# Optimization experiments

Hardware: AMD Instinct MI355X
Metric: run time of the kernel (lower is better)

Reference implementation:

```python
import jax, jax.numpy as jnp
import numpy as np

B, N = 32, 512            # batch, max nodes per graph
F_DIM, M_DIM = 1024, 256  # node feature dim, first hidden dim
N_SEM = 8                 # number of semantic-class experts
XYZ, DIM_E = 3, 8
OUT_SIZE = 2 * XYZ + DIM_E  # 14 (default reg branch)
EPS = 1e-8                # padding value used by out_seq_to_batch


def setup_inputs() -> dict:
    key = jax.random.key(0)
    ks = jax.random.split(key, 12)
    def w(k, shape, fan_in):
        return jax.random.normal(k, shape, jnp.float32) / np.float32(np.sqrt(fan_in))
    return {
        "nodes": jax.random.normal(ks[0], (B, N, F_DIM), jnp.float32),
        "sem": jax.random.randint(ks[1], (B, N), 0, N_SEM, jnp.int32),
        "lengths": jax.random.randint(ks[2], (B,), 64, N + 1, jnp.int32),
        # y expert MLPs (4 layers), stacked over experts
        "W1": w(ks[3], (N_SEM, F_DIM, M_DIM), F_DIM), "b1": jnp.zeros((N_SEM, M_DIM), jnp.float32),
        "W2": w(ks[4], (N_SEM, M_DIM, 64), M_DIM),   "b2": jnp.zeros((N_SEM, 64), jnp.float32),
        "W3": w(ks[5], (N_SEM, 64, 32), 64),         "b3": jnp.zeros((N_SEM, 32), jnp.float32),
        "W4": w(ks[6], (N_SEM, 32, OUT_SIZE), 32),   "b4": jnp.zeros((N_SEM, OUT_SIZE), jnp.float32),
        # rot expert MLPs (2 layers), stacked over experts
        "R1": w(ks[7], (N_SEM, F_DIM, M_DIM), F_DIM), "rb1": jnp.zeros((N_SEM, M_DIM), jnp.float32),
        "R2": w(ks[8], (N_SEM, M_DIM, XYZ), M_DIM),   "rb2": jnp.zeros((N_SEM, XYZ), jnp.float32),
    }


def _prim_mlps(nodes, sem, lengths, W1, b1, W2, b2, W3, b3, W4, b4, R1, rb1, R2, rb2):
    Bn, Nn, Fd = nodes.shape
    x = nodes.reshape(-1, Fd)                       # [T, F], T = B*N tokens
    semf = sem.reshape(-1)                          # [T] expert id per token
    # dense dispatch: run every expert on all tokens, then select per token
    h1 = jax.nn.relu(jnp.einsum('tf,efm->etm', x, W1) + b1[:, None, :])   # [E,T,M]
    h2 = jax.nn.relu(jnp.einsum('etm,emh->eth', h1, W2) + b2[:, None, :]) # [E,T,64]
    h3 = jax.nn.relu(jnp.einsum('eth,ehg->etg', h2, W3) + b3[:, None, :]) # [E,T,32]
    y_all = jnp.einsum('etg,ego->eto', h3, W4) + b4[:, None, :]           # [E,T,OUT]
    r1 = jax.nn.relu(jnp.einsum('tf,efm->etm', x, R1) + rb1[:, None, :])  # [E,T,M]
    rot_all = jnp.einsum('etm,emo->eto', r1, R2) + rb2[:, None, :]        # [E,T,XYZ]
    t = jnp.arange(x.shape[0])
    y = y_all[semf, t]                              # [T, OUT]
    rot = rot_all[semf, t]                          # [T, XYZ]
    out = jnp.concatenate([y, rot], axis=-1).reshape(Bn, Nn, -1)
    # positions beyond each graph's length are filled with eps (out_seq_to_batch)
    mask = (jnp.arange(Nn)[None, :] < lengths[:, None])[:, :, None]
    return jnp.where(mask, out, jnp.float32(EPS))


def reference(nodes, sem, lengths, W1, b1, W2, b2, W3, b3, W4, b4, R1, rb1, R2, rb2):
    return _prim_mlps(nodes, sem, lengths, W1, b1, W2, b2, W3, b3, W4, b4,
                      R1, rb1, R2, rb2)
```

## Files before the change

### kernel.cpp

```cpp
#include <hip/hip_runtime.h>
#include <stdint.h>

#define T_TOK 16384
#define NE 8
#define EPSV 1e-8f
#define MAXC128 136
#define MAXC64  264

#define WS_PERM   0
#define WS_CNT    65536
#define WS_CUR    65600
#define WS_OFFS   65664
#define WS_XS     131072
#define WS_WT     (WS_XS + 16512*1024*2)
#define WS_H1     (WS_WT + 8*512*1024*2)
#define WS_W2T    (WS_H1 + 16448*512*2)
#define WS_W3T    (WS_W2T + 8*64*256*2)
#define WS_W4T    (WS_W3T + 8*32*64*2)
#define WS_R2T    (WS_W4T + 8*16*32*2)

typedef __attribute__((ext_vector_type(8))) short bf16x8;
typedef __attribute__((ext_vector_type(4))) float f32x4;

__device__ __forceinline__ unsigned short f2bf(float f) {
    unsigned u = __float_as_uint(f);
    u += 0x7fffu + ((u >> 16) & 1u);
    return (unsigned short)(u >> 16);
}
__device__ __forceinline__ float bf2f(unsigned short h) {
    return __uint_as_float(((unsigned)h) << 16);
}

__device__ __forceinline__ void gl_lds16(const void* g, void* l) {
    __builtin_amdgcn_global_load_lds(
        (const __attribute__((address_space(1))) void*)g,
        (__attribute__((address_space(3))) void*)l,
        16, 0, 0);
}

__device__ __forceinline__ bool chunk_lookup(const int* __restrict__ offs, int c, int csize,
                                             int& e, int& base, int& len) {
    int acc = 0;
#pragma unroll
    for (int i = 0; i < NE; i++) {
        int s = offs[i], t = offs[i + 1];
        int cc = (t - s + csize - 1) / csize;
        if (c < acc + cc) {
            e = i;
            base = s + (c - acc) * csize;
            len = (t - base < csize) ? (t - base) : csize;
            return true;
        }
        acc += cc;
    }
    return false;
}

__global__ __launch_bounds__(64) void k_zero(int* __restrict__ ws_i) {
    int t = threadIdx.x;
    if (t < NE) ws_i[(WS_CNT >> 2) + t] = 0;
    if (t < NE) ws_i[(WS_CUR >> 2) + t] = 0;
}

__global__ __launch_bounds__(256) void k_hist(const int* __restrict__ sem, int* __restrict__ ws_i) {
    __shared__ int cnt[NE];
    int tid = threadIdx.x, lane = tid & 63;
    if (tid < NE) cnt[tid] = 0;
    __syncthreads();
    int s = sem[blockIdx.x * 256 + tid];
#pragma unroll
    for (int e = 0; e < NE; e++) {
        unsigned long long m = __ballot(s == e);
        if (lane == e) atomicAdd(&cnt[e], (int)__popcll(m));
    }
    __syncthreads();
    if (tid < NE) atomicAdd(ws_i + (WS_CNT >> 2) + tid, cnt[tid]);
}

__global__ __launch_bounds__(64) void k_scan(int* __restrict__ ws_i) {
    if (threadIdx.x == 0) {
        int acc = 0;
        int* offs = ws_i + (WS_OFFS >> 2);
        for (int e = 0; e < NE; e++) {
            offs[e] = acc;
            ws_i[(WS_CUR >> 2) + e] = acc;
            acc += ws_i[(WS_CNT >> 2) + e];
        }
        offs[NE] = acc;
    }
}

__global__ __launch_bounds__(256) void k_scatter(const int* __restrict__ sem, int* __restrict__ ws_i) {
    int tid = threadIdx.x, lane = tid & 63;
    int i = blockIdx.x * 256 + tid;
    int s = sem[i];
    int* perm = ws_i + (WS_PERM >> 2);
#pragma unroll
    for (int e = 0; e < NE; e++) {
        unsigned long long m = __ballot(s == e);
        if (s == e) {
            int leader = (int)__builtin_ctzll(m);
            int rank = (int)__popcll(m & ((1ull << lane) - 1ull));
            int bpos = 0;
            if (lane == leader) bpos = atomicAdd(ws_i + (WS_CUR >> 2) + e, (int)__popcll(m));
            bpos = __shfl(bpos, leader, 64);
            perm[bpos + rank] = i;
        }
    }
}

__global__ __launch_bounds__(256) void k_xgather(const float* __restrict__ x,
                                                 const int* __restrict__ perm,
                                                 unsigned short* __restrict__ xs) {
    int gid = blockIdx.x * 256 + threadIdx.x;
    int st = gid >> 7;
    int k8 = gid & 127;
    int src = perm[st];
    const float4* p = (const float4*)(x + (size_t)src * 1024 + k8 * 8);
    float4 a = p[0], b = p[1];
    unsigned r0 = (unsigned)f2bf(a.x) | ((unsigned)f2bf(a.y) << 16);
    unsigned r1 = (unsigned)f2bf(a.z) | ((unsigned)f2bf(a.w) << 16);
    unsigned r2 = (unsigned)f2bf(b.x) | ((unsigned)f2bf(b.y) << 16);
    unsigned r3 = (unsigned)f2bf(b.z) | ((unsigned)f2bf(b.w) << 16);
    *(uint4*)(xs + (size_t)st * 1024 + k8 * 8) = make_uint4(r0, r1, r2, r3);
}

__global__ __launch_bounds__(256) void k_wcvt(const float* __restrict__ W1,
                                              const float* __restrict__ R1,
                                              unsigned short* __restrict__ wt) {
    __shared__ float tile[64][65];
    int k0 = blockIdx.x * 64;
    int n0 = blockIdx.y * 64;
    int e  = blockIdx.z;
    const float* src = (n0 < 256) ? (W1 + (size_t)e * 1024 * 256 + n0)
                                  : (R1 + (size_t)e * 1024 * 256 + (n0 - 256));
    int tid = threadIdx.x;
    int rr = tid >> 4;
    int cg = (tid & 15) * 4;
#pragma unroll
    for (int p = 0; p < 4; p++) {
        int kk = p * 16 + rr;
        float4 v = *(const float4*)(src + (size_t)(k0 + kk) * 256 + cg);
        tile[kk][cg] = v.x; tile[kk][cg + 1] = v.y; tile[kk][cg + 2] = v.z; tile[kk][cg + 3] = v.w;
    }
    __syncthreads();
    int nn = tid >> 3;
    int k8 = tid & 7;
#pragma unroll
    for (int p = 0; p < 2; p++) {
        int n = p * 32 + nn;
        unsigned w[4];
#pragma unroll
        for (int j = 0; j < 4; j++) {
            float f0 = tile[k8 * 8 + 2 * j][n];
            float f1 = tile[k8 * 8 + 2 * j + 1][n];
            w[j] = (unsigned)f2bf(f0) | ((unsigned)f2bf(f1) << 16);
        }
        *(uint4*)(wt + (size_t)(e * 512 + n0 + n) * 1024 + k0 + k8 * 8) =
            make_uint4(w[0], w[1], w[2], w[3]);
    }
}

__global__ __launch_bounds__(256) void k_wcvt2(const float* __restrict__ W2,
                                               const float* __restrict__ W3,
                                               const float* __restrict__ W4,
                                               const float* __restrict__ R2,
                                               unsigned short* __restrict__ w2t,
                                               unsigned short* __restrict__ w3t,
                                               unsigned short* __restrict__ w4t,
                                               unsigned short* __restrict__ r2t) {
    int e = blockIdx.x, t = threadIdx.x;
    for (int idx = t; idx < 64 * 256; idx += 256) {
        int k = idx & 255, n = idx >> 8;
        w2t[(size_t)(e * 64 + n) * 256 + k] = f2bf(W2[(size_t)e * 16384 + k * 64 + n]);
    }
    for (int idx = t; idx < 32 * 64; idx += 256) {
        int k = idx & 63, n = idx >> 6;
        w3t[(size_t)(e * 32 + n) * 64 + k] = f2bf(W3[(size_t)e * 2048 + k * 32 + n]);
    }
    for (int idx = t; idx < 16 * 32; idx += 256) {
        int k = idx & 31, n = idx >> 5;
        w4t[(size_t)(e * 16 + n) * 32 + k] = (n < 14) ? f2bf(W4[(size_t)e * 448 + k * 14 + n])
                                                      : (unsigned short)0;
    }
    for (int idx = t; idx < 16 * 256; idx += 256) {
        int k = idx & 255, n = idx >> 8;
        r2t[(size_t)(e * 16 + n) * 256 + k] = (n < 3) ? f2bf(R2[(size_t)e * 768 + k * 3 + n])
                                                      : (unsigned short)0;
    }
}

__global__ __launch_bounds__(256) void k_gemm(const unsigned short* __restrict__ xs,
                                              const unsigned short* __restrict__ wt,
                                              const float* __restrict__ b1,
                                              const float* __restrict__ rb1,
                                              const int* __restrict__ ws_i,
                                              unsigned short* __restrict__ h1) {
    __shared__ __align__(16) short As[128 * 32];
    __shared__ __align__(16) short Bs[128 * 32];
    int e, base, len;
    if (!chunk_lookup(ws_i + (WS_OFFS >> 2), blockIdx.x, 128, e, base, len)) return;
    int n0 = blockIdx.y * 128;
    int tid = threadIdx.x;
    int wave = tid >> 6, lane = tid & 63;
    int quad = lane >> 4, lr = lane & 15;
    int wm = (wave & 1) * 64, wn = (wave >> 1) * 64;

    f32x4 acc[4][4];
#pragma unroll
    for (int i = 0; i < 4; i++)
#pragma unroll
        for (int j = 0; j < 4; j++) acc[i][j] = (f32x4){0.f, 0.f, 0.f, 0.f};

    const unsigned short* Ag = xs + (size_t)base * 1024;
    const unsigned short* Bg = wt + (size_t)(e * 512 + n0) * 1024;

    for (int kb = 0; kb < 32; kb++) {
        __syncthreads();
#pragma unroll
        for (int i = 0; i < 2; i++) {
            int g = i * 256 + wave * 64 + lane;
            int r = g >> 2, k8 = g & 3;
            gl_lds16(Ag + (size_t)r * 1024 + kb * 32 + k8 * 8,
                     As + (size_t)(i * 256 + wave * 64) * 8);
            gl_lds16(Bg + (size_t)r * 1024 + kb * 32 + k8 * 8,
                     Bs + (size_t)(i * 256 + wave * 64) * 8);
        }
        __syncthreads();

        bf16x8 af[4], bfr[4];
#pragma unroll
        for (int im = 0; im < 4; im++)
            af[im] = *(const bf16x8*)(As + ((wm + im * 16 + lr) * 32 + quad * 8));
#pragma unroll
        for (int in = 0; in < 4; in++)
            bfr[in] = *(const bf16x8*)(Bs + ((wn + in * 16 + lr) * 32 + quad * 8));
#pragma unroll
        for (int im = 0; im < 4; im++)
#pragma unroll
            for (int in = 0; in < 4; in++)
                acc[im][in] = __builtin_amdgcn_mfma_f32_16x16x32_bf16(af[im], bfr[in], acc[im][in], 0, 0, 0);
    }

#pragma unroll
    for (int in = 0; in < 4; in++) {
        int gcol = n0 + wn + in * 16 + lr;
        float bias = (gcol < 256) ? b1[e * 256 + gcol] : rb1[e * 256 + gcol - 256];
#pragma unroll
        for (int im = 0; im < 4; im++) {
#pragma unroll
            for (int v = 0; v < 4; v++) {
                int r = wm + im * 16 + quad * 4 + v;
                if (r < len) {
                    float val = fmaxf(acc[im][in][v] + bias, 0.f);
                    h1[(size_t)(base + r) * 512 + gcol] = f2bf(val);
                }
            }
        }
    }
}

__global__ __launch_bounds__(256) void k_tail(const unsigned short* __restrict__ h1,
                                              const int* __restrict__ ws_i,
                                              const unsigned short* __restrict__ w2t,
                                              const unsigned short* __restrict__ w3t,
                                              const unsigned short* __restrict__ w4t,
                                              const unsigned short* __restrict__ r2t,
                                              const float* __restrict__ b2,
                                              const float* __restrict__ b3,
                                              const float* __restrict__ b4,
                                              const float* __restrict__ rb2,
                                              const int* __restrict__ lengths,
                                              float* __restrict__ out) {
    __shared__ __align__(16) unsigned short h2s[4][16][64];
    __shared__ __align__(16) unsigned short h3s[4][16][32];

    int e, base, len;
    if (!chunk_lookup(ws_i + (WS_OFFS >> 2), blockIdx.x, 64, e, base, len)) return;
    int tid = threadIdx.x, wave = tid >> 6, lane = tid & 63;
    int quad = lane >> 4, lr = lane & 15;
    int m0 = wave * 16;

    const unsigned short* Ap = h1 + (size_t)(base + m0) * 512;

    f32x4 acc2[4];
#pragma unroll
    for (int t = 0; t < 4; t++) {
        float bb = b2[e * 64 + t * 16 + lr];
        acc2[t] = (f32x4){bb, bb, bb, bb};
    }
    f32x4 accr;
    { float bb = (lr < 3) ? rb2[e * 3 + lr] : 0.f; accr = (f32x4){bb, bb, bb, bb}; }

    const unsigned short* W2e = w2t + (size_t)e * 64 * 256;
    const unsigned short* R2e = r2t + (size_t)e * 16 * 256;
#pragma unroll
    for (int kk = 0; kk < 8; kk++) {
        int k0 = kk * 32;
        bf16x8 a = *(const bf16x8*)(Ap + lr * 512 + k0 + quad * 8);
#pragma unroll
        for (int t = 0; t < 4; t++) {
            bf16x8 b = *(const bf16x8*)(W2e + (t * 16 + lr) * 256 + k0 + quad * 8);
            acc2[t] = __builtin_amdgcn_mfma_f32_16x16x32_bf16(a, b, acc2[t], 0, 0, 0);
        }
        bf16x8 ar = *(const bf16x8*)(Ap + lr * 512 + 256 + k0 + quad * 8);
        bf16x8 br = *(const bf16x8*)(R2e + lr * 256 + k0 + quad * 8);
        accr = __builtin_amdgcn_mfma_f32_16x16x32_bf16(ar, br, accr, 0, 0, 0);
    }
#pragma unroll
    for (int t = 0; t < 4; t++)
#pragma unroll
        for (int v = 0; v < 4; v++)
            h2s[wave][quad * 4 + v][t * 16 + lr] = f2bf(fmaxf(acc2[t][v], 0.f));

    f32x4 acc3[2];
#pragma unroll
    for (int t = 0; t < 2; t++) {
        float bb = b3[e * 32 + t * 16 + lr];
        acc3[t] = (f32x4){bb, bb, bb, bb};
    }
    const unsigned short* W3e = w3t + (size_t)e * 32 * 64;
#pragma unroll
    for (int kk = 0; kk < 2; kk++) {
        int k0 = kk * 32;
        bf16x8 a = *(const bf16x8*)(&h2s[wave][lr][k0 + quad * 8]);
#pragma unroll
        for (int t = 0; t < 2; t++) {
            bf16x8 b = *(const bf16x8*)(W3e + (t * 16 + lr) * 64 + k0 + quad * 8);
            acc3[t] = __builtin_amdgcn_mfma_f32_16x16x32_bf16(a, b, acc3[t], 0, 0, 0);
        }
    }
#pragma unroll
    for (int t = 0; t < 2; t++)
#pragma unroll
        for (int v = 0; v < 4; v++)
            h3s[wave][quad * 4 + v][t * 16 + lr] = f2bf(fmaxf(acc3[t][v], 0.f));

    f32x4 acc4;
    { float bb = (lr < 14) ? b4[e * 14 + lr] : 0.f; acc4 = (f32x4){bb, bb, bb, bb}; }
    {
        bf16x8 a = *(const bf16x8*)(&h3s[wave][lr][quad * 8]);
        bf16x8 b = *(const bf16x8*)(w4t + ((size_t)e * 16 + lr) * 32 + quad * 8);
        acc4 = __builtin_amdgcn_mfma_f32_16x16x32_bf16(a, b, acc4, 0, 0, 0);
    }

    const int* perm = ws_i + (WS_PERM >> 2);
#pragma unroll
    for (int v = 0; v < 4; v++) {
        int t = m0 + quad * 4 + v;
        if (t < len) {
            int token = perm[base + t];
            int bi = token >> 9, ni = token & 511;
            int valid = ni < lengths[bi];
            if (lr < 14) out[(size_t)token * 17 + lr] = valid ? acc4[v] : EPSV;
            if (lr < 3)  out[(size_t)token * 17 + 14 + lr] = valid ? accr[v] : EPSV;
        }
    }
}

extern "C" void kernel_launch(void* const* d_in, const int* in_sizes, int n_in,
                              void* d_out, int out_size, void* d_ws, size_t ws_size,
                              hipStream_t stream) {
    (void)in_sizes; (void)n_in; (void)out_size; (void)ws_size;
    const float* nodes   = (const float*)d_in[0];
    const int*   sem     = (const int*)d_in[1];
    const int*   lengths = (const int*)d_in[2];
    const float* W1 = (const float*)d_in[3];
    const float* b1 = (const float*)d_in[4];
    const float* W2 = (const float*)d_in[5];
    const float* b2 = (const float*)d_in[6];
    const float* W3 = (const float*)d_in[7];
    const float* b3 = (const float*)d_in[8];
    const float* W4 = (const float*)d_in[9];
    const float* b4 = (const float*)d_in[10];
    const float* R1  = (const float*)d_in[11];
    const float* rb1 = (const float*)d_in[12];
    const float* R2  = (const float*)d_in[13];
    const float* rb2 = (const float*)d_in[14];
    float* out = (float*)d_out;

    char* ws = (char*)d_ws;
    int* ws_i = (int*)ws;
    unsigned short* xs  = (unsigned short*)(ws + WS_XS);
    unsigned short* wt  = (unsigned short*)(ws + WS_WT);
    unsigned short* h1  = (unsigned short*)(ws + WS_H1);
    unsigned short* w2t = (unsigned short*)(ws + WS_W2T);
    unsigned short* w3t = (unsigned short*)(ws + WS_W3T);
    unsigned short* w4t = (unsigned short*)(ws + WS_W4T);
    unsigned short* r2t = (unsigned short*)(ws + WS_R2T);

    hipLaunchKernelGGL(k_zero, dim3(1), dim3(64), 0, stream, ws_i);
    hipLaunchKernelGGL(k_hist, dim3(64), dim3(256), 0, stream, sem, ws_i);
    hipLaunchKernelGGL(k_scan, dim3(1), dim3(64), 0, stream, ws_i);
    hipLaunchKernelGGL(k_scatter, dim3(64), dim3(256), 0, stream, sem, ws_i);
    hipLaunchKernelGGL(k_xgather, dim3(8192), dim3(256), 0, stream, nodes, (const int*)ws_i, xs);
    hipLaunchKernelGGL(k_wcvt, dim3(16, 8, 8), dim3(256), 0, stream, W1, R1, wt);
    hipLaunchKernelGGL(k_wcvt2, dim3(8), dim3(256), 0, stream, W2, W3, W4, R2, w2t, w3t, w4t, r2t);
    hipLaunchKernelGGL(k_gemm, dim3(MAXC128, 4), dim3(256), 0, stream,
                       (const unsigned short*)xs, (const unsigned short*)wt, b1, rb1,
                       (const int*)ws_i, h1);
    hipLaunchKernelGGL(k_tail, dim3(MAXC64), dim3(256), 0, stream,
                       (const unsigned short*)h1, (const int*)ws_i,
                       (const unsigned short*)w2t, (const unsigned short*)w3t,
                       (const unsigned short*)w4t, (const unsigned short*)r2t,
                       b2, b3, b4, rb2, lengths, out);
}
```

Before: 236.0 us.

## Cut launches via per-block hist partials, fuse weight converts, widen GEMM K tile

Per-block histogram partials are written out, and each scatter block computes its own expert offsets from them. This removes the zero and scan kernels and the global atomics on cursors. The small-weight conversion is folded into the W1/R1 conversion kernel, spread across its blocks, so one more launch goes away. The first-layer GEMM now loads 64-wide K tiles with an XOR-swizzled LDS layout, halving the number of K iterations and barriers and reducing bank conflicts, at the cost of doubled LDS per block.

```diff
diff --git a/kernel.cpp b/kernel.cpp
--- a/kernel.cpp
+++ b/kernel.cpp
@@ -8,9 +8,8 @@
 #define MAXC64  264
 
 #define WS_PERM   0
-#define WS_CNT    65536
-#define WS_CUR    65600
-#define WS_OFFS   65664
+#define WS_PART   65536
+#define WS_OFFS   67584
 #define WS_XS     131072
 #define WS_WT     (WS_XS + 16512*1024*2)
 #define WS_H1     (WS_WT + 8*512*1024*2)
@@ -56,12 +55,6 @@
     return false;
 }
 
-__global__ __launch_bounds__(64) void k_zero(int* __restrict__ ws_i) {
-    int t = threadIdx.x;
-    if (t < NE) ws_i[(WS_CNT >> 2) + t] = 0;
-    if (t < NE) ws_i[(WS_CUR >> 2) + t] = 0;
-}
-
 __global__ __launch_bounds__(256) void k_hist(const int* __restrict__ sem, int* __restrict__ ws_i) {
     __shared__ int cnt[NE];
     int tid = threadIdx.x, lane = tid & 63;
@@ -74,25 +67,38 @@
         if (lane == e) atomicAdd(&cnt[e], (int)__popcll(m));
     }
     __syncthreads();
-    if (tid < NE) atomicAdd(ws_i + (WS_CNT >> 2) + tid, cnt[tid]);
-}
-
-__global__ __launch_bounds__(64) void k_scan(int* __restrict__ ws_i) {
-    if (threadIdx.x == 0) {
-        int acc = 0;
-        int* offs = ws_i + (WS_OFFS >> 2);
-        for (int e = 0; e < NE; e++) {
-            offs[e] = acc;
-            ws_i[(WS_CUR >> 2) + e] = acc;
-            acc += ws_i[(WS_CNT >> 2) + e];
-        }
-        offs[NE] = acc;
-    }
+    if (tid < NE) ws_i[(WS_PART >> 2) + blockIdx.x * NE + tid] = cnt[tid];
 }
 
 __global__ __launch_bounds__(256) void k_scatter(const int* __restrict__ sem, int* __restrict__ ws_i) {
-    int tid = threadIdx.x, lane = tid & 63;
-    int i = blockIdx.x * 256 + tid;
+    __shared__ int parts[64 * NE];
+    __shared__ int tot[NE], preb[NE], ebase[NE + 1];
+    __shared__ int cur[NE];
+    int b = blockIdx.x, tid = threadIdx.x, lane = tid & 63;
+    parts[tid] = ws_i[(WS_PART >> 2) + tid];
+    parts[256 + tid] = ws_i[(WS_PART >> 2) + 256 + tid];
+    __syncthreads();
+    if (tid < NE) {
+        int t = 0, p = 0;
+        for (int bb = 0; bb < 64; bb++) {
+            int v = parts[bb * NE + tid];
+            t += v;
+            if (bb < b) p += v;
+        }
+        tot[tid] = t; preb[tid] = p;
+    }
+    __syncthreads();
+    if (tid == 0) {
+        int base = 0;
+        for (int e = 0; e < NE; e++) { ebase[e] = base; base += tot[e]; }
+        ebase[NE] = base;
+        if (b == 0)
+            for (int e = 0; e <= NE; e++) ws_i[(WS_OFFS >> 2) + e] = ebase[e];
+    }
+    __syncthreads();
+    if (tid < NE) cur[tid] = ebase[tid] + preb[tid];
+    __syncthreads();
+    int i = b * 256 + tid;
     int s = sem[i];
     int* perm = ws_i + (WS_PERM >> 2);
 #pragma unroll
@@ -102,7 +108,7 @@
             int leader = (int)__builtin_ctzll(m);
             int rank = (int)__popcll(m & ((1ull << lane) - 1ull));
             int bpos = 0;
-            if (lane == leader) bpos = atomicAdd(ws_i + (WS_CUR >> 2) + e, (int)__popcll(m));
+            if (lane == leader) bpos = atomicAdd(&cur[e], (int)__popcll(m));
             bpos = __shfl(bpos, leader, 64);
             perm[bpos + rank] = i;
         }
@@ -127,7 +133,15 @@
 
 __global__ __launch_bounds__(256) void k_wcvt(const float* __restrict__ W1,
                                               const float* __restrict__ R1,
-                                              unsigned short* __restrict__ wt) {
+                                              const float* __restrict__ W2,
+                                              const float* __restrict__ W3,
+                                              const float* __restrict__ W4,
+                                              const float* __restrict__ R2,
+                                              unsigned short* __restrict__ wt,
+                                              unsigned short* __restrict__ w2t,
+                                              unsigned short* __restrict__ w3t,
+                                              unsigned short* __restrict__ w4t,
+                                              unsigned short* __restrict__ r2t) {
     __shared__ float tile[64][65];
     int k0 = blockIdx.x * 64;
     int n0 = blockIdx.y * 64;
@@ -159,34 +173,26 @@
         *(uint4*)(wt + (size_t)(e * 512 + n0 + n) * 1024 + k0 + k8 * 8) =
             make_uint4(w[0], w[1], w[2], w[3]);
     }
-}
-
-__global__ __launch_bounds__(256) void k_wcvt2(const float* __restrict__ W2,
-                                               const float* __restrict__ W3,
-                                               const float* __restrict__ W4,
-                                               const float* __restrict__ R2,
-                                               unsigned short* __restrict__ w2t,
-                                               unsigned short* __restrict__ w3t,
-                                               unsigned short* __restrict__ w4t,
-                                               unsigned short* __restrict__ r2t) {
-    int e = blockIdx.x, t = threadIdx.x;
-    for (int idx = t; idx < 64 * 256; idx += 256) {
-        int k = idx & 255, n = idx >> 8;
-        w2t[(size_t)(e * 64 + n) * 256 + k] = f2bf(W2[(size_t)e * 16384 + k * 64 + n]);
-    }
-    for (int idx = t; idx < 32 * 64; idx += 256) {
-        int k = idx & 63, n = idx >> 6;
-        w3t[(size_t)(e * 32 + n) * 64 + k] = f2bf(W3[(size_t)e * 2048 + k * 32 + n]);
-    }
-    for (int idx = t; idx < 16 * 32; idx += 256) {
-        int k = idx & 31, n = idx >> 5;
-        w4t[(size_t)(e * 16 + n) * 32 + k] = (n < 14) ? f2bf(W4[(size_t)e * 448 + k * 14 + n])
-                                                      : (unsigned short)0;
-    }
-    for (int idx = t; idx < 16 * 256; idx += 256) {
-        int k = idx & 255, n = idx >> 8;
-        r2t[(size_t)(e * 16 + n) * 256 + k] = (n < 3) ? f2bf(R2[(size_t)e * 768 + k * 3 + n])
-                                                      : (unsigned short)0;
+    if (blockIdx.y == 0) {
+        int x = blockIdx.x;
+        for (int j = tid; j < 1024; j += 256) {
+            int idx = x * 1024 + j; int k = idx & 255, n = idx >> 8;
+            w2t[(size_t)(e * 64 + n) * 256 + k] = f2bf(W2[(size_t)e * 16384 + k * 64 + n]);
+        }
+        if (tid < 128) {
+            int idx = x * 128 + tid; int k = idx & 63, n = idx >> 6;
+            w3t[(size_t)(e * 32 + n) * 64 + k] = f2bf(W3[(size_t)e * 2048 + k * 32 + n]);
+        }
+        if (tid < 32) {
+            int idx = x * 32 + tid; int k = idx & 31, n = idx >> 5;
+            w4t[(size_t)(e * 16 + n) * 32 + k] = (n < 14) ? f2bf(W4[(size_t)e * 448 + k * 14 + n])
+                                                          : (unsigned short)0;
+        }
+        {
+            int idx = x * 256 + tid; int k = idx & 255, n = idx >> 8;
+            r2t[(size_t)(e * 16 + n) * 256 + k] = (n < 3) ? f2bf(R2[(size_t)e * 768 + k * 3 + n])
+                                                          : (unsigned short)0;
+        }
     }
 }
 
@@ -196,8 +202,8 @@
                                               const float* __restrict__ rb1,
                                               const int* __restrict__ ws_i,
                                               unsigned short* __restrict__ h1) {
-    __shared__ __align__(16) short As[128 * 32];
-    __shared__ __align__(16) short Bs[128 * 32];
+    __shared__ __align__(16) short As[128 * 64];
+    __shared__ __align__(16) short Bs[128 * 64];
     int e, base, len;
     if (!chunk_lookup(ws_i + (WS_OFFS >> 2), blockIdx.x, 128, e, base, len)) return;
     int n0 = blockIdx.y * 128;
@@ -215,31 +221,54 @@
     const unsigned short* Ag = xs + (size_t)base * 1024;
     const unsigned short* Bg = wt + (size_t)(e * 512 + n0) * 1024;
 
-    for (int kb = 0; kb < 32; kb++) {
+    const unsigned short* srcA[4];
+    const unsigned short* srcB[4];
+    int dst[4];
+#pragma unroll
+    for (int i = 0; i < 4; i++) {
+        int s = i * 256 + wave * 64 + lane;
+        int r = s >> 3, c = s & 7;
+        int cs = c ^ (r & 7);
+        srcA[i] = Ag + (size_t)r * 1024 + cs * 8;
+        srcB[i] = Bg + (size_t)r * 1024 + cs * 8;
+        dst[i] = (i * 256 + wave * 64) * 8;
+    }
+
+    for (int kb = 0; kb < 16; kb++) {
         __syncthreads();
 #pragma unroll
-        for (int i = 0; i < 2; i++) {
-            int g = i * 256 + wave * 64 + lane;
-            int r = g >> 2, k8 = g & 3;
-            gl_lds16(Ag + (size_t)r * 1024 + kb * 32 + k8 * 8,
-                     As + (size_t)(i * 256 + wave * 64) * 8);
-            gl_lds16(Bg + (size_t)r * 1024 + kb * 32 + k8 * 8,
-                     Bs + (size_t)(i * 256 + wave * 64) * 8);
+        for (int i = 0; i < 4; i++) {
+            gl_lds16(srcA[i] + kb * 64, As + dst[i]);
+            gl_lds16(srcB[i] + kb * 64, Bs + dst[i]);
         }
         __syncthreads();
 
-        bf16x8 af[4], bfr[4];
-#pragma unroll
-        for (int im = 0; im < 4; im++)
-            af[im] = *(const bf16x8*)(As + ((wm + im * 16 + lr) * 32 + quad * 8));
-#pragma unroll
-        for (int in = 0; in < 4; in++)
-            bfr[in] = *(const bf16x8*)(Bs + ((wn + in * 16 + lr) * 32 + quad * 8));
-#pragma unroll
-        for (int im = 0; im < 4; im++)
-#pragma unroll
-            for (int in = 0; in < 4; in++)
-                acc[im][in] = __builtin_amdgcn_mfma_f32_16x16x32_bf16(af[im], bfr[in], acc[im][in], 0, 0, 0);
+        bf16x8 af[2][4], bfr[2][4];
+#pragma unroll
+        for (int im = 0; im < 4; im++) {
+            int r = wm + im * 16 + lr;
+#pragma unroll
+            for (int kh = 0; kh < 2; kh++) {
+                int q = kh * 4 + quad;
+                af[kh][im] = *(const bf16x8*)(As + (r * 8 + (q ^ (r & 7))) * 8);
+            }
+        }
+#pragma unroll
+        for (int in = 0; in < 4; in++) {
+            int r = wn + in * 16 + lr;
+#pragma unroll
+            for (int kh = 0; kh < 2; kh++) {
+                int q = kh * 4 + quad;
+                bfr[kh][in] = *(const bf16x8*)(Bs + (r * 8 + (q ^ (r & 7))) * 8);
+            }
+        }
+#pragma unroll
+        for (int kh = 0; kh < 2; kh++)
+#pragma unroll
+            for (int im = 0; im < 4; im++)
+#pragma unroll
+                for (int in = 0; in < 4; in++)
+                    acc[im][in] = __builtin_amdgcn_mfma_f32_16x16x32_bf16(af[kh][im], bfr[kh][in], acc[im][in], 0, 0, 0);
     }
 
 #pragma unroll
@@ -389,13 +418,11 @@
     unsigned short* w4t = (unsigned short*)(ws + WS_W4T);
     unsigned short* r2t = (unsigned short*)(ws + WS_R2T);
 
-    hipLaunchKernelGGL(k_zero, dim3(1), dim3(64), 0, stream, ws_i);
     hipLaunchKernelGGL(k_hist, dim3(64), dim3(256), 0, stream, sem, ws_i);
-    hipLaunchKernelGGL(k_scan, dim3(1), dim3(64), 0, stream, ws_i);
     hipLaunchKernelGGL(k_scatter, dim3(64), dim3(256), 0, stream, sem, ws_i);
     hipLaunchKernelGGL(k_xgather, dim3(8192), dim3(256), 0, stream, nodes, (const int*)ws_i, xs);
-    hipLaunchKernelGGL(k_wcvt, dim3(16, 8, 8), dim3(256), 0, stream, W1, R1, wt);
-    hipLaunchKernelGGL(k_wcvt2, dim3(8), dim3(256), 0, stream, W2, W3, W4, R2, w2t, w3t, w4t, r2t);
+    hipLaunchKernelGGL(k_wcvt, dim3(16, 8, 8), dim3(256), 0, stream,
+                       W1, R1, W2, W3, W4, R2, wt, w2t, w3t, w4t, r2t);
     hipLaunchKernelGGL(k_gemm, dim3(MAXC128, 4), dim3(256), 0, stream,
                        (const unsigned short*)xs, (const unsigned short*)wt, b1, rb1,
                        (const int*)ws_i, h1);
```

New measurement: 204.2 us. 13.5% less time.
